# Optimization experiments

Hardware: AMD Instinct MI355X
Metric: run time of the kernel (lower is better)

The kernel has to match this reference:

```python
import jax, jax.numpy as jnp
import numpy as np

B, S, D = 4096, 200, 64
H1, H2 = 80, 40


def setup_inputs() -> dict:
    key = jax.random.key(0)
    ks = jax.random.split(key, 9)
    seq = jax.random.normal(ks[0], (B, S, D), dtype=jnp.float32)
    tgt = jax.random.normal(ks[1], (B, D), dtype=jnp.float32)
    mask = jax.random.randint(ks[2], (B, S), 0, 2, dtype=jnp.int32)
    # MLP params: (4*D -> H1 -> H2 -> 1), glorot-ish init
    def lin(k, fan_in, fan_out):
        s = (2.0 / (fan_in + fan_out)) ** 0.5
        return jax.random.normal(k, (fan_in, fan_out), dtype=jnp.float32) * s
    W1 = lin(ks[3], 4 * D, H1)
    b1 = jnp.zeros((H1,), dtype=jnp.float32)
    W2 = lin(ks[4], H1, H2)
    b2 = jnp.zeros((H2,), dtype=jnp.float32)
    W3 = lin(ks[5], H2, 1)
    b3 = jnp.zeros((1,), dtype=jnp.float32)
    return {"sequence_emb": seq, "target_emb": tgt, "mask": mask,
            "W1": W1, "b1": b1, "W2": W2, "b2": b2, "W3": W3, "b3": b3}


def reference(sequence_emb, target_emb, mask, W1, b1, W2, b2, W3, b3):
    # DIN attention: concat[target, seq, target-seq, target*seq] -> MLP -> mask -> softmax
    t = target_emb[:, None, :]                                   # [B,1,D] broadcast over S
    t_full = jnp.broadcast_to(t, sequence_emb.shape)             # [B,S,D]
    din = jnp.concatenate(
        [t_full, sequence_emb, t_full - sequence_emb, t_full * sequence_emb],
        axis=-1)                                                 # [B,S,4D]
    h = jax.nn.relu(jnp.einsum('bsi,ij->bsj', din, W1) + b1)     # [B,S,H1]
    h = jax.nn.relu(jnp.einsum('bsi,ij->bsj', h, W2) + b2)       # [B,S,H2]
    score = (jnp.einsum('bsi,ij->bsj', h, W3) + b3)[..., 0]      # [B,S]
    m = mask.astype(score.dtype)
    score = score * m + (-1e9) * (1.0 - m)
    return jax.nn.softmax(score, axis=-1)
```

## Files before the change

### kernel.cpp

```cpp
#include <hip/hip_runtime.h>
#include <hip/hip_bf16.h>


#define WS_WCT   0
#define WS_W2T   20480
#define WS_B2P   29696
#define WS_W3P   29888
#define WS_U     30080

typedef __attribute__((ext_vector_type(8))) short short8;
typedef __attribute__((ext_vector_type(4))) float f32x4;

static __device__ __forceinline__ unsigned short f2bf(float f) {
    unsigned int u = __builtin_bit_cast(unsigned int, f);
    u = (u + 0x7FFFu + ((u >> 16) & 1u)) >> 16;
    return (unsigned short)u;
}

static __device__ __forceinline__ short8 pk8(float4 a, float4 b) {
    short8 r;
    r[0] = (short)f2bf(a.x); r[1] = (short)f2bf(a.y);
    r[2] = (short)f2bf(a.z); r[3] = (short)f2bf(a.w);
    r[4] = (short)f2bf(b.x); r[5] = (short)f2bf(b.y);
    r[6] = (short)f2bf(b.z); r[7] = (short)f2bf(b.w);
    return r;
}

#define FENCE() do { asm volatile("s_waitcnt lgkmcnt(0)" ::: "memory"); \
                     __builtin_amdgcn_sched_barrier(0); } while (0)

__global__ __launch_bounds__(256) void prep_w_kernel(
    const float* __restrict__ W1, const float* __restrict__ W2,
    const float* __restrict__ b2, const float* __restrict__ W3,
    unsigned char* __restrict__ ws)
{
    const int tid = threadIdx.x;
    unsigned short* wcT = (unsigned short*)(ws + WS_WCT);
    for (int idx = tid; idx < 80 * 128; idx += 256) {
        int c = idx >> 7, k = idx & 127;
        float v;
        if (k < 64) v = W1[(64 + k) * 80 + c] - W1[(128 + k) * 80 + c];
        else        v = W1[(192 + (k - 64)) * 80 + c];
        wcT[(c << 7) + (k ^ ((c & 7) << 3))] = f2bf(v);
    }
    unsigned short* w2T = (unsigned short*)(ws + WS_W2T);
    for (int idx = tid; idx < 48 * 96; idx += 256) {
        int c = idx / 96, k = idx % 96;
        float v = (c < 40 && k < 80) ? W2[k * 40 + c] : 0.0f;
        w2T[idx] = f2bf(v);
    }
    float* b2p = (float*)(ws + WS_B2P);
    float* w3p = (float*)(ws + WS_W3P);
    for (int idx = tid; idx < 48; idx += 256) {
        b2p[idx] = (idx < 40) ? b2[idx] : 0.0f;
        w3p[idx] = (idx < 40) ? W3[idx] : 0.0f;
    }
    float* Uf = (float*)(ws + WS_U);
    for (int idx = tid; idx < 64 * 80; idx += 256) {
        int d = idx / 80, h = idx - d * 80;
        Uf[idx] = W1[d * 80 + h] + W1[(128 + d) * 80 + h];
    }
}

__global__ __launch_bounds__(256, 2) void score_kernel(
    const float* __restrict__ seq, const float* __restrict__ tgt,
    const float* __restrict__ b1g, const unsigned char* __restrict__ ws,
    float* __restrict__ out)
{
    __shared__ __align__(16) unsigned char w1s[20480];
    __shared__ __align__(16) float Us[5120];
    __shared__ __align__(16) unsigned char slots[4][4096];

    const int tid = threadIdx.x;
    {
        const float4* s1 = (const float4*)(ws + WS_WCT);
        float4* d1 = (float4*)w1s;
        const float4* s2 = (const float4*)(ws + WS_U);
        float4* d2 = (float4*)Us;
        #pragma unroll
        for (int i = 0; i < 5; ++i) {
            d1[tid + 256 * i] = s1[tid + 256 * i];
            d2[tid + 256 * i] = s2[tid + 256 * i];
        }
        float4 z = {0.f, 0.f, 0.f, 0.f};
        float4* sz = (float4*)slots;
        #pragma unroll
        for (int i = 0; i < 4; ++i) sz[tid + 256 * i] = z;
    }
    __syncthreads();

    const int l  = tid & 63;
    const int w  = tid >> 6;
    const int cb = l & 15;
    const int kq = l >> 4;
    const int swi = (cb & 7) << 4;

    const unsigned short* w2T = (const unsigned short*)(ws + WS_W2T);
    short8 bL2[3][3];
    #pragma unroll
    for (int kt = 0; kt < 3; ++kt)
        #pragma unroll
        for (int mt = 0; mt < 3; ++mt)
            bL2[kt][mt] = *(const short8*)(w2T + (cb + 16 * mt) * 96 + kt * 32 + kq * 8);
    const float* b2p = (const float*)(ws + WS_B2P);
    const float* w3p = (const float*)(ws + WS_W3P);
    float bw[3][4], wv[3][4];
    #pragma unroll
    for (int mt = 0; mt < 3; ++mt)
        #pragma unroll
        for (int j = 0; j < 4; ++j) {
            int c2 = mt * 16 + kq * 4 + j;
            bw[mt][j] = b2p[c2]; wv[mt][j] = w3p[c2];
        }

    unsigned char* slot = slots[w];
    const int gw = blockIdx.x * 4 + w;
    const int bA = gw * 2;
    int tau = gw * 26;

    float biasA[5], biasB[5];
    #pragma unroll
    for (int nt = 0; nt < 5; ++nt) {
        float v0 = b1g[nt * 16 + cb];
        biasA[nt] = v0; biasB[nt] = v0;
    }
    for (int d = 0; d < 64; ++d) {
        float tA = tgt[bA * 64 + d];
        float tB = tgt[bA * 64 + 64 + d];
        #pragma unroll
        for (int nt = 0; nt < 5; ++nt) {
            float u = Us[d * 80 + nt * 16 + cb];
            biasA[nt] += tA * u; biasB[nt] += tB * u;
        }
    }

#define STAGE(TAU, S0,S1,S2,S3, T0,T1,T2,T3) do {                              \
        int tc = (TAU); tc = tc > 53247 ? 53247 : tc;                          \
        int b_ = tc / 13; int tt_ = tc - b_ * 13;                              \
        int row = tt_ * 16 + cb; row = row > 199 ? 199 : row;                  \
        const float* sp = seq + ((size_t)b_ * 200 + row) * 64 + kq * 8;        \
        S0 = *(const float4*)sp;        S1 = *(const float4*)(sp + 4);         \
        S2 = *(const float4*)(sp + 32); S3 = *(const float4*)(sp + 36);        \
        const float* tp = tgt + (size_t)b_ * 64 + kq * 8;                      \
        T0 = *(const float4*)tp;        T1 = *(const float4*)(tp + 4);         \
        T2 = *(const float4*)(tp + 32); T3 = *(const float4*)(tp + 36);        \
    } while (0)

#define PROCESS(TAU, S0,S1,S2,S3, T0,T1,T2,T3) do {                            \
        int b_ = (TAU) / 13; int tt_ = (TAU) - b_ * 13;                        \
        float biasc_[5];                                                       \
        _Pragma("unroll")                                                      \
        for (int nt = 0; nt < 5; ++nt)                                         \
            biasc_[nt] = (b_ == bA) ? biasA[nt] : biasB[nt];                   \
        short8 a0 = pk8(S0, S1), a1 = pk8(S2, S3);                             \
        short8 a2 = pk8(T0 * S0, T1 * S1), a3 = pk8(T2 * S2, T3 * S3);         \
        f32x4 acc[5] = {};                                                     \
        _Pragma("unroll")                                                      \
        for (int kt = 0; kt < 4; ++kt) {                                       \
            short8 av = kt == 0 ? a0 : kt == 1 ? a1 : kt == 2 ? a2 : a3;       \
            _Pragma("unroll")                                                  \
            for (int nt = 0; nt < 5; ++nt) {                                   \
                short8 bf = *(const short8*)(w1s + (cb + 16 * nt) * 256 +      \
                                             ((kt * 64 + kq * 16) ^ swi));     \
                acc[nt] = __builtin_amdgcn_mfma_f32_16x16x32_bf16(av, bf, acc[nt], 0, 0, 0); \
            }                                                                  \
        }                                                                      \
        _Pragma("unroll")                                                      \
        for (int nt = 0; nt < 5; ++nt)                                         \
            _Pragma("unroll")                                                  \
            for (int j = 0; j < 4; ++j) {                                      \
                float h = fmaxf(acc[nt][j] + biasc_[nt], 0.0f);                \
                int r = kq * 4 + j, c = nt * 16 + cb;                          \
                *(unsigned short*)(slot + r * 256 + ((2 * c) ^ ((r & 7) << 4))) = f2bf(h); \
            }                                                                  \
        FENCE();                                                               \
        f32x4 acc2[3] = {};                                                    \
        _Pragma("unroll")                                                      \
        for (int kt = 0; kt < 3; ++kt) {                                       \
            short8 hf = *(const short8*)(slot + cb * 256 +                     \
                                         ((kt * 64 + kq * 16) ^ swi));         \
            _Pragma("unroll")                                                  \
            for (int mt = 0; mt < 3; ++mt)                                     \
                acc2[mt] = __builtin_amdgcn_mfma_f32_16x16x32_bf16(bL2[kt][mt], hf, acc2[mt], 0, 0, 0); \
        }                                                                      \
        float part = 0.0f;                                                     \
        _Pragma("unroll")                                                      \
        for (int mt = 0; mt < 3; ++mt)                                         \
            _Pragma("unroll")                                                  \
            for (int j = 0; j < 4; ++j)                                        \
                part += fmaxf(acc2[mt][j] + bw[mt][j], 0.0f) * wv[mt][j];      \
        part += __shfl_xor(part, 16, 64);                                      \
        part += __shfl_xor(part, 32, 64);                                      \
        if (l < 16) {                                                          \
            int row = tt_ * 16 + cb;                                           \
            if (row < 200) out[(size_t)b_ * 200 + row] = part;                 \
        }                                                                      \
    } while (0)

    float4 sa0, sa1, sa2, sa3, ta0, ta1, ta2, ta3;
    float4 sb0, sb1, sb2, sb3, tb0, tb1, tb2, tb3;
    STAGE(tau, sa0, sa1, sa2, sa3, ta0, ta1, ta2, ta3);
    for (int i = 0; i < 13; ++i) {
        STAGE(tau + 1, sb0, sb1, sb2, sb3, tb0, tb1, tb2, tb3);
        PROCESS(tau,    sa0, sa1, sa2, sa3, ta0, ta1, ta2, ta3);
        STAGE(tau + 2, sa0, sa1, sa2, sa3, ta0, ta1, ta2, ta3);
        PROCESS(tau + 1, sb0, sb1, sb2, sb3, tb0, tb1, tb2, tb3);
        tau += 2;
    }
}

__global__ __launch_bounds__(256) void softmax_kernel(
    const int* __restrict__ mask, float* __restrict__ out)
{
    const int l = threadIdx.x & 63;
    const int w = threadIdx.x >> 6;
    const int b = blockIdx.x * 4 + w;
    float* po = out + (size_t)b * 200;
    const int* pm = mask + (size_t)b * 200;
    float v[4];
    #pragma unroll
    for (int j = 0; j < 4; ++j) {
        int tk = l + 64 * j;
        v[j] = (tk < 200) ? (pm[tk] ? po[tk] : -1.0e9f) : -3.0e38f;
    }
    float mx = fmaxf(fmaxf(v[0], v[1]), fmaxf(v[2], v[3]));
    #pragma unroll
    for (int st = 32; st >= 1; st >>= 1) mx = fmaxf(mx, __shfl_xor(mx, st, 64));
    float e[4], sm = 0.0f;
    #pragma unroll
    for (int j = 0; j < 4; ++j) {
        int tk = l + 64 * j;
        e[j] = (tk < 200) ? expf(v[j] - mx) : 0.0f;
        sm += e[j];
    }
    #pragma unroll
    for (int st = 32; st >= 1; st >>= 1) sm += __shfl_xor(sm, st, 64);
    float inv = 1.0f / sm;
    #pragma unroll
    for (int j = 0; j < 4; ++j) {
        int tk = l + 64 * j;
        if (tk < 200) po[tk] = e[j] * inv;
    }
}

extern "C" void kernel_launch(void* const* d_in, const int* in_sizes, int n_in,
                              void* d_out, int out_size, void* d_ws, size_t ws_size,
                              hipStream_t stream)
{
    const float* seq = (const float*)d_in[0];
    const float* tgt = (const float*)d_in[1];
    const int*   msk = (const int*)d_in[2];
    const float* W1  = (const float*)d_in[3];
    const float* b1  = (const float*)d_in[4];
    const float* W2  = (const float*)d_in[5];
    const float* b2  = (const float*)d_in[6];
    const float* W3  = (const float*)d_in[7];
    unsigned char* ws = (unsigned char*)d_ws;
    float* out = (float*)d_out;

    prep_w_kernel<<<1, 256, 0, stream>>>(W1, W2, b2, W3, ws);
    score_kernel<<<512, 256, 0, stream>>>(seq, tgt, b1, ws, out);
    softmax_kernel<<<1024, 256, 0, stream>>>(msk, out);
}
```

Before: 78.71 us.

## Fuse masked softmax into score kernel with one batch row per wave

Each wave now owns exactly one batch row, so the target vector and the folded first-layer bias are loaded once per wave instead of per tile. Per-row scores are kept in shared memory and the masked softmax runs in the same kernel, which removes the separate softmax launch and its round trip of scores through global memory. The U matrix is no longer copied to LDS, which frees shared memory so more blocks can fit per CU (launch bounds raised to 4). In exchange each wave handles fewer tiles, so the shorter prefetch chain gives it fewer chances to hide memory latency, and the kernel launches twice as many blocks.

```diff
diff --git a/kernel.cpp b/kernel.cpp
--- a/kernel.cpp
+++ b/kernel.cpp
@@ -62,38 +62,33 @@
     }
 }
 
-__global__ __launch_bounds__(256, 2) void score_kernel(
+__global__ __launch_bounds__(256, 4) void score_kernel(
     const float* __restrict__ seq, const float* __restrict__ tgt,
-    const float* __restrict__ b1g, const unsigned char* __restrict__ ws,
-    float* __restrict__ out)
+    const int* __restrict__ mask, const float* __restrict__ b1g,
+    const unsigned char* __restrict__ ws, float* __restrict__ out)
 {
     __shared__ __align__(16) unsigned char w1s[20480];
-    __shared__ __align__(16) float Us[5120];
     __shared__ __align__(16) unsigned char slots[4][4096];
+    __shared__ float scStash[4][13][16];
 
     const int tid = threadIdx.x;
     {
         const float4* s1 = (const float4*)(ws + WS_WCT);
         float4* d1 = (float4*)w1s;
-        const float4* s2 = (const float4*)(ws + WS_U);
-        float4* d2 = (float4*)Us;
-        #pragma unroll
-        for (int i = 0; i < 5; ++i) {
-            d1[tid + 256 * i] = s1[tid + 256 * i];
-            d2[tid + 256 * i] = s2[tid + 256 * i];
-        }
+        #pragma unroll
+        for (int i = 0; i < 5; ++i) d1[tid + 256 * i] = s1[tid + 256 * i];
         float4 z = {0.f, 0.f, 0.f, 0.f};
         float4* sz = (float4*)slots;
         #pragma unroll
         for (int i = 0; i < 4; ++i) sz[tid + 256 * i] = z;
     }
-    __syncthreads();
 
     const int l  = tid & 63;
     const int w  = tid >> 6;
     const int cb = l & 15;
     const int kq = l >> 4;
     const int swi = (cb & 7) << 4;
+    const int b  = blockIdx.x * 4 + w;
 
     const unsigned short* w2T = (const unsigned short*)(ws + WS_W2T);
     short8 bL2[3][3];
@@ -113,45 +108,36 @@
             bw[mt][j] = b2p[c2]; wv[mt][j] = w3p[c2];
         }
 
+    const float* tp = tgt + (size_t)b * 64 + kq * 8;
+    const float4 T0 = *(const float4*)tp;        const float4 T1 = *(const float4*)(tp + 4);
+    const float4 T2 = *(const float4*)(tp + 32); const float4 T3 = *(const float4*)(tp + 36);
+
+    float biasA[5];
+    #pragma unroll
+    for (int nt = 0; nt < 5; ++nt) biasA[nt] = b1g[nt * 16 + cb];
+    {
+        const float* Uf = (const float*)(ws + WS_U);
+        const float* tb = tgt + (size_t)b * 64;
+        #pragma unroll 4
+        for (int d = 0; d < 64; ++d) {
+            float tA = tb[d];
+            #pragma unroll
+            for (int nt = 0; nt < 5; ++nt)
+                biasA[nt] += tA * Uf[d * 80 + nt * 16 + cb];
+        }
+    }
+    __syncthreads();
+
     unsigned char* slot = slots[w];
-    const int gw = blockIdx.x * 4 + w;
-    const int bA = gw * 2;
-    int tau = gw * 26;
-
-    float biasA[5], biasB[5];
-    #pragma unroll
-    for (int nt = 0; nt < 5; ++nt) {
-        float v0 = b1g[nt * 16 + cb];
-        biasA[nt] = v0; biasB[nt] = v0;
-    }
-    for (int d = 0; d < 64; ++d) {
-        float tA = tgt[bA * 64 + d];
-        float tB = tgt[bA * 64 + 64 + d];
-        #pragma unroll
-        for (int nt = 0; nt < 5; ++nt) {
-            float u = Us[d * 80 + nt * 16 + cb];
-            biasA[nt] += tA * u; biasB[nt] += tB * u;
-        }
-    }
-
-#define STAGE(TAU, S0,S1,S2,S3, T0,T1,T2,T3) do {                              \
-        int tc = (TAU); tc = tc > 53247 ? 53247 : tc;                          \
-        int b_ = tc / 13; int tt_ = tc - b_ * 13;                              \
-        int row = tt_ * 16 + cb; row = row > 199 ? 199 : row;                  \
-        const float* sp = seq + ((size_t)b_ * 200 + row) * 64 + kq * 8;        \
+
+#define STAGE(TT, S0,S1,S2,S3) do {                                            \
+        int row = (TT) * 16 + cb; row = row > 199 ? 199 : row;                 \
+        const float* sp = seq + ((size_t)b * 200 + row) * 64 + kq * 8;         \
         S0 = *(const float4*)sp;        S1 = *(const float4*)(sp + 4);         \
         S2 = *(const float4*)(sp + 32); S3 = *(const float4*)(sp + 36);        \
-        const float* tp = tgt + (size_t)b_ * 64 + kq * 8;                      \
-        T0 = *(const float4*)tp;        T1 = *(const float4*)(tp + 4);         \
-        T2 = *(const float4*)(tp + 32); T3 = *(const float4*)(tp + 36);        \
     } while (0)
 
-#define PROCESS(TAU, S0,S1,S2,S3, T0,T1,T2,T3) do {                            \
-        int b_ = (TAU) / 13; int tt_ = (TAU) - b_ * 13;                        \
-        float biasc_[5];                                                       \
-        _Pragma("unroll")                                                      \
-        for (int nt = 0; nt < 5; ++nt)                                         \
-            biasc_[nt] = (b_ == bA) ? biasA[nt] : biasB[nt];                   \
+#define PROCESS(TT, S0,S1,S2,S3) do {                                          \
         short8 a0 = pk8(S0, S1), a1 = pk8(S2, S3);                             \
         short8 a2 = pk8(T0 * S0, T1 * S1), a3 = pk8(T2 * S2, T3 * S3);         \
         f32x4 acc[5] = {};                                                     \
@@ -169,7 +155,7 @@
         for (int nt = 0; nt < 5; ++nt)                                         \
             _Pragma("unroll")                                                  \
             for (int j = 0; j < 4; ++j) {                                      \
-                float h = fmaxf(acc[nt][j] + biasc_[nt], 0.0f);                \
+                float h = fmaxf(acc[nt][j] + biasA[nt], 0.0f);                 \
                 int r = kq * 4 + j, c = nt * 16 + cb;                          \
                 *(unsigned short*)(slot + r * 256 + ((2 * c) ^ ((r & 7) << 4))) = f2bf(h); \
             }                                                                  \
@@ -191,55 +177,47 @@
                 part += fmaxf(acc2[mt][j] + bw[mt][j], 0.0f) * wv[mt][j];      \
         part += __shfl_xor(part, 16, 64);                                      \
         part += __shfl_xor(part, 32, 64);                                      \
-        if (l < 16) {                                                          \
-            int row = tt_ * 16 + cb;                                           \
-            if (row < 200) out[(size_t)b_ * 200 + row] = part;                 \
-        }                                                                      \
+        if (l < 16) scStash[w][TT][cb] = part;                                 \
+        FENCE();                                                               \
     } while (0)
 
-    float4 sa0, sa1, sa2, sa3, ta0, ta1, ta2, ta3;
-    float4 sb0, sb1, sb2, sb3, tb0, tb1, tb2, tb3;
-    STAGE(tau, sa0, sa1, sa2, sa3, ta0, ta1, ta2, ta3);
-    for (int i = 0; i < 13; ++i) {
-        STAGE(tau + 1, sb0, sb1, sb2, sb3, tb0, tb1, tb2, tb3);
-        PROCESS(tau,    sa0, sa1, sa2, sa3, ta0, ta1, ta2, ta3);
-        STAGE(tau + 2, sa0, sa1, sa2, sa3, ta0, ta1, ta2, ta3);
-        PROCESS(tau + 1, sb0, sb1, sb2, sb3, tb0, tb1, tb2, tb3);
-        tau += 2;
-    }
-}
-
-__global__ __launch_bounds__(256) void softmax_kernel(
-    const int* __restrict__ mask, float* __restrict__ out)
-{
-    const int l = threadIdx.x & 63;
-    const int w = threadIdx.x >> 6;
-    const int b = blockIdx.x * 4 + w;
-    float* po = out + (size_t)b * 200;
-    const int* pm = mask + (size_t)b * 200;
-    float v[4];
-    #pragma unroll
-    for (int j = 0; j < 4; ++j) {
-        int tk = l + 64 * j;
-        v[j] = (tk < 200) ? (pm[tk] ? po[tk] : -1.0e9f) : -3.0e38f;
-    }
-    float mx = fmaxf(fmaxf(v[0], v[1]), fmaxf(v[2], v[3]));
-    #pragma unroll
-    for (int st = 32; st >= 1; st >>= 1) mx = fmaxf(mx, __shfl_xor(mx, st, 64));
-    float e[4], sm = 0.0f;
-    #pragma unroll
-    for (int j = 0; j < 4; ++j) {
-        int tk = l + 64 * j;
-        e[j] = (tk < 200) ? expf(v[j] - mx) : 0.0f;
-        sm += e[j];
-    }
-    #pragma unroll
-    for (int st = 32; st >= 1; st >>= 1) sm += __shfl_xor(sm, st, 64);
+    float4 sa0, sa1, sa2, sa3;
+    float4 sb0, sb1, sb2, sb3;
+    STAGE(0, sa0, sa1, sa2, sa3);
+    #pragma unroll 1
+    for (int i = 0; i < 6; ++i) {
+        STAGE(2 * i + 1, sb0, sb1, sb2, sb3);
+        PROCESS(2 * i,     sa0, sa1, sa2, sa3);
+        STAGE(2 * i + 2, sa0, sa1, sa2, sa3);
+        PROCESS(2 * i + 1, sb0, sb1, sb2, sb3);
+    }
+    PROCESS(12, sa0, sa1, sa2, sa3);
+
+    float vv[13];
+    #pragma unroll
+    for (int tt = 0; tt < 13; ++tt) {
+        int row = tt * 16 + cb;
+        int mk = (row < 200) ? mask[(size_t)b * 200 + row] : 0;
+        float sc = scStash[w][tt][cb];
+        vv[tt] = mk ? sc : ((row < 200) ? -1.0e9f : -3.0e38f);
+    }
+    float mx = -3.0e38f;
+    #pragma unroll
+    for (int tt = 0; tt < 13; ++tt) mx = fmaxf(mx, vv[tt]);
+    #pragma unroll
+    for (int st = 1; st < 16; st <<= 1) mx = fmaxf(mx, __shfl_xor(mx, st, 64));
+    float ee[13], sm = 0.0f;
+    #pragma unroll
+    for (int tt = 0; tt < 13; ++tt) { ee[tt] = __expf(vv[tt] - mx); sm += ee[tt]; }
+    #pragma unroll
+    for (int st = 1; st < 16; st <<= 1) sm += __shfl_xor(sm, st, 64);
     float inv = 1.0f / sm;
     #pragma unroll
-    for (int j = 0; j < 4; ++j) {
-        int tk = l + 64 * j;
-        if (tk < 200) po[tk] = e[j] * inv;
+    for (int tt = 0; tt < 13; ++tt) {
+        if ((tt & 3) == kq) {
+            int row = tt * 16 + cb;
+            if (row < 200) out[(size_t)b * 200 + row] = ee[tt] * inv;
+        }
     }
 }
 
@@ -259,6 +237,5 @@
     float* out = (float*)d_out;
 
     prep_w_kernel<<<1, 256, 0, stream>>>(W1, W2, b2, W3, ws);
-    score_kernel<<<512, 256, 0, stream>>>(seq, tgt, b1, ws, out);
-    softmax_kernel<<<1024, 256, 0, stream>>>(msk, out);
-}
+    score_kernel<<<1024, 256, 0, stream>>>(seq, tgt, msk, b1, ws, out);
+}
```

Result: slower. 208.8 us (+165.3%).
